# Optimization experiments

Hardware: AMD Instinct MI355X
Metric: run time of the kernel (lower is better)

The kernel has to match this reference:

```python
import jax, jax.numpy as jnp
import numpy as np

H = 16
D_MODEL = 1024
D_K = D_MODEL // H


def setup_inputs() -> dict:
    key = jax.random.key(0)
    ks = jax.random.split(key, 11)
    B, S = 2, 2048
    scale = 1.0 / np.sqrt(D_MODEL)
    inp = {
        "query": jax.random.normal(ks[0], (B, S, D_MODEL), dtype=jnp.float32),
        "key": jax.random.normal(ks[1], (B, S, D_MODEL), dtype=jnp.float32),
        "value": jax.random.normal(ks[2], (B, S, D_MODEL), dtype=jnp.float32),
        "Wq": jax.random.normal(ks[3], (D_MODEL, D_MODEL), dtype=jnp.float32) * scale,
        "bq": jnp.zeros((D_MODEL,), dtype=jnp.float32),
        "Wk": jax.random.normal(ks[4], (D_MODEL, D_MODEL), dtype=jnp.float32) * scale,
        "bk": jnp.zeros((D_MODEL,), dtype=jnp.float32),
        "Wv": jax.random.normal(ks[5], (D_MODEL, D_MODEL), dtype=jnp.float32) * scale,
        "bv": jnp.zeros((D_MODEL,), dtype=jnp.float32),
        "Wo": jax.random.normal(ks[6], (D_MODEL, D_MODEL), dtype=jnp.float32) * scale,
        "bo": jnp.zeros((D_MODEL,), dtype=jnp.float32),
    }
    return inp


def _mha(query, key, value, Wq, bq, Wk, bk, Wv, bv, Wo, bo):
    B, S, _ = query.shape
    # linear projections (torch nn.Linear: x @ W.T + b)
    q = query @ Wq.T + bq
    k = key @ Wk.T + bk
    v = value @ Wv.T + bv
    # split heads: [B, S, D] -> [B, H, S, d_k]
    q = q.reshape(B, S, H, D_K).transpose(0, 2, 1, 3)
    k = k.reshape(B, S, H, D_K).transpose(0, 2, 1, 3)
    v = v.reshape(B, S, H, D_K).transpose(0, 2, 1, 3)
    # scaled dot-product attention with manual stable softmax
    scores = jnp.einsum("bhqd,bhkd->bhqk", q, k) / jnp.sqrt(jnp.float32(D_K))
    stable = scores - jnp.max(scores, axis=-1, keepdims=True)
    e = jnp.exp(stable)
    attn = e / jnp.sum(e, axis=-1, keepdims=True)
    ctx = jnp.einsum("bhqk,bhkd->bhqd", attn, v)
    # merge heads and final projection
    ctx = ctx.transpose(0, 2, 1, 3).reshape(B, S, H * D_K)
    return ctx @ Wo.T + bo


def reference(query, key, value, Wq, bq, Wk, bk, Wv, bv, Wo, bo):
    return _mha(query, key, value, Wq, bq, Wk, bk, Wv, bv, Wo, bo)
```

## Files before the change

### kernel.cpp

```cpp
#include <hip/hip_runtime.h>


#define S_LEN 2048
#define BATCH 2
#define DM    1024
#define NH    16
#define DKH   64
#define BS    (BATCH * S_LEN)

typedef _Float16 f16x8 __attribute__((ext_vector_type(8)));
typedef _Float16 f16x4 __attribute__((ext_vector_type(4)));
typedef _Float16 f16x2 __attribute__((ext_vector_type(2)));
typedef __fp16   h16x2 __attribute__((ext_vector_type(2)));
typedef float    f32x4 __attribute__((ext_vector_type(4)));

__device__ __forceinline__ f16x2 pk_f16(float a, float b) {
  h16x2 r = __builtin_amdgcn_cvt_pkrtz(a, b);
  return __builtin_bit_cast(f16x2, r);
}

__device__ __forceinline__ void gld16(const void* g, void* l) {
  __builtin_amdgcn_global_load_lds(
      (const __attribute__((address_space(1))) void*)g,
      (__attribute__((address_space(3))) void*)l, 16, 0, 0);
}

__device__ __forceinline__ float fast_exp2(float x) {
#if __has_builtin(__builtin_amdgcn_exp2f)
  return __builtin_amdgcn_exp2f(x);
#else
  return exp2f(x);
#endif
}

__global__ __launch_bounds__(256) void cvt_all(
    const float* __restrict__ q, const float* __restrict__ k, const float* __restrict__ v,
    const float* __restrict__ wq, const float* __restrict__ wk,
    const float* __restrict__ wv, const float* __restrict__ wo,
    _Float16* __restrict__ xq, _Float16* __restrict__ xk, _Float16* __restrict__ xv,
    _Float16* __restrict__ w16)
{
  const int y = blockIdx.y;
  const float* src; _Float16* dst; int n;
  if (y == 0)      { src = q;  dst = xq; n = BS * DM; }
  else if (y == 1) { src = k;  dst = xk; n = BS * DM; }
  else if (y == 2) { src = v;  dst = xv; n = BS * DM; }
  else {
    src = (y == 3) ? wq : ((y == 4) ? wk : ((y == 5) ? wv : wo));
    dst = w16 + (size_t)(y - 3) * (DM * DM);
    n = DM * DM;
  }
  int i0 = (blockIdx.x * 256 + threadIdx.x) * 4;
  if (i0 < n) {
    float4 f = *(const float4*)(src + i0);
    f16x2 lo = pk_f16(f.x, f.y);
    f16x2 hi = pk_f16(f.z, f.w);
    f16x4 h; h[0] = lo[0]; h[1] = lo[1]; h[2] = hi[0]; h[3] = hi[1];
    *(f16x4*)(dst + i0) = h;
  }
}

template <typename OUT_T, bool VT>
__device__ __forceinline__ void gemm_core(
    const _Float16* __restrict__ A, const _Float16* __restrict__ W,
    const float* __restrict__ bias, OUT_T* __restrict__ out, float oscale)
{
  const int tid  = threadIdx.x;
  const int l    = tid & 63;
  const int wv   = tid >> 6;
  const int c    = l & 15, quad = l >> 4;
  const int m0   = blockIdx.y * 128, n0 = blockIdx.x * 128;
  const int wm   = wv & 1, wn = wv >> 1;
  __shared__ _Float16 sA[128 * 64];
  __shared__ _Float16 sB[128 * 64];

  const _Float16* gA[4]; const _Float16* gB[4];
#pragma unroll
  for (int p = 0; p < 4; ++p) {
    int s = tid + p * 256, r = s >> 3, g = (s & 7) ^ (r & 7);
    gA[p] = A + (size_t)(m0 + r) * DM + g * 8;
    gB[p] = W + (size_t)(n0 + r) * DM + g * 8;
  }
  const int cx = c & 7;

  f32x4 acc[4][4] = {};
  for (int k0 = 0; k0 < DM; k0 += 64) {
    __syncthreads();
#pragma unroll
    for (int p = 0; p < 4; ++p) {
      gld16(gA[p] + k0, sA + (tid + p * 256) * 8);
      gld16(gB[p] + k0, sB + (tid + p * 256) * 8);
    }
    __syncthreads();
#pragma unroll
    for (int ks = 0; ks < 2; ++ks) {
      f16x8 af[4], bf[4];
#pragma unroll
      for (int i = 0; i < 4; ++i)
        af[i] = *(const f16x8*)&sA[(wm * 64 + i * 16 + c) * 64 + ((ks * 4 + quad) ^ cx) * 8];
#pragma unroll
      for (int j = 0; j < 4; ++j)
        bf[j] = *(const f16x8*)&sB[(wn * 64 + j * 16 + c) * 64 + ((ks * 4 + quad) ^ cx) * 8];
#pragma unroll
      for (int i = 0; i < 4; ++i)
#pragma unroll
        for (int j = 0; j < 4; ++j)
          acc[i][j] = __builtin_amdgcn_mfma_f32_16x16x32_f16(af[i], bf[j], acc[i][j], 0, 0, 0);
    }
  }
  if constexpr (VT) {
#pragma unroll
    for (int j = 0; j < 4; ++j) {
      int col = n0 + wn * 64 + j * 16 + c;
      float bb = bias[col];
      int hh = col >> 6, dd = col & 63;
#pragma unroll
      for (int i = 0; i < 4; ++i) {
        int row = m0 + wm * 64 + i * 16 + quad * 4;
        int bb2 = row >> 11, ss = row & (S_LEN - 1);
        _Float16* dst = (_Float16*)out + ((size_t)(bb2 * NH + hh) * DKH + dd) * S_LEN + ss;
        f16x4 v4;
#pragma unroll
        for (int r = 0; r < 4; ++r) v4[r] = (_Float16)((acc[i][j][r] + bb) * oscale);
        *(f16x4*)dst = v4;
      }
    }
  } else {
#pragma unroll
    for (int j = 0; j < 4; ++j) {
      int col = n0 + wn * 64 + j * 16 + c;
      float bb = bias[col];
#pragma unroll
      for (int i = 0; i < 4; ++i) {
        int row = m0 + wm * 64 + i * 16 + quad * 4;
#pragma unroll
        for (int r = 0; r < 4; ++r) {
          float vv = (acc[i][j][r] + bb) * oscale;
          out[(size_t)(row + r) * DM + col] = (OUT_T)vv;
        }
      }
    }
  }
}

#define SC_Q (0.125f * 1.44269504088896340736f)

__global__ __launch_bounds__(256) void proj3(
    const _Float16* __restrict__ xq, const _Float16* __restrict__ xk,
    const _Float16* __restrict__ xv, const _Float16* __restrict__ w16,
    const float* __restrict__ bq, const float* __restrict__ bk, const float* __restrict__ bv,
    _Float16* __restrict__ Q, _Float16* __restrict__ K, _Float16* __restrict__ Vt)
{
  const int z = blockIdx.z;
  if (z == 2) {
    gemm_core<_Float16, true>(xv, w16 + (size_t)2 * DM * DM, bv, Vt, 1.0f);
  } else if (z == 0) {
    gemm_core<_Float16, false>(xq, w16, bq, Q, SC_Q);
  } else {
    gemm_core<_Float16, false>(xk, w16 + (size_t)DM * DM, bk, K, 1.0f);
  }
}

__global__ __launch_bounds__(256) void out_gemm(
    const _Float16* __restrict__ ctx, const _Float16* __restrict__ wo,
    const float* __restrict__ bo, float* __restrict__ out)
{
  gemm_core<float, false>(ctx, wo, bo, out, 1.0f);
}

#define APP 72
__global__ __launch_bounds__(256) void attn(
    const _Float16* __restrict__ Q, const _Float16* __restrict__ K,
    const _Float16* __restrict__ Vt, _Float16* __restrict__ ctx)
{
  const int tid = threadIdx.x;
  const int l   = tid & 63, wv = tid >> 6;
  const int c   = l & 15, quad = l >> 4;
  const int q0  = blockIdx.x * 64;
  const int bh  = blockIdx.y;
  const int b   = bh >> 4, h = bh & 15;
  const int wq  = wv & 1, wd = wv >> 1;
  __shared__ _Float16 sK[64 * 64];
  __shared__ _Float16 sV[64 * 64];
  __shared__ _Float16 sP[64 * APP];
  __shared__ float    lsum[64][4];

  f16x8 qf[4][2];
#pragma unroll
  for (int nt = 0; nt < 4; ++nt) {
    const _Float16* Qg = Q + ((size_t)(b * S_LEN + q0 + nt * 16 + c)) * DM + h * DKH;
    qf[nt][0] = *(const f16x8*)(Qg + quad * 8);
    qf[nt][1] = *(const f16x8*)(Qg + 32 + quad * 8);
  }

  f32x4 o[2][2] = {};
  float l_part[4] = {};

  const _Float16* Kg0 = K + ((size_t)b * S_LEN) * DM + h * DKH;
  const _Float16* Vg0 = Vt + ((size_t)bh * DKH) * S_LEN;

  const int sa = tid,       ra = sa >> 3, ba = (sa & 7) ^ (ra & 7);
  const int sb = tid + 256, rb = sb >> 3, bb = (sb & 7) ^ (rb & 7);
  const _Float16* gKa = Kg0 + (size_t)ra * DM + ba * 8;
  const _Float16* gKb = Kg0 + (size_t)rb * DM + bb * 8;
  const _Float16* gVa = Vg0 + (size_t)ra * S_LEN + ba * 8;
  const _Float16* gVb = Vg0 + (size_t)rb * S_LEN + bb * 8;
  const int cx = c & 7;

  for (int kt = 0; kt < S_LEN / 64; ++kt) {
    const int k0 = kt * 64;
    __syncthreads();
    gld16(gKa + (size_t)k0 * DM, sK + sa * 8);
    gld16(gKb + (size_t)k0 * DM, sK + sb * 8);
    gld16(gVa + k0,              sV + sa * 8);
    gld16(gVb + k0,              sV + sb * 8);
    __syncthreads();

    f32x4 sAcc[4] = {};
#pragma unroll
    for (int ks = 0; ks < 2; ++ks) {
      f16x8 kf = *(const f16x8*)&sK[(wv * 16 + c) * 64 + ((ks * 4 + quad) ^ cx) * 8];
#pragma unroll
      for (int nt = 0; nt < 4; ++nt)
        sAcc[nt] = __builtin_amdgcn_mfma_f32_16x16x32_f16(kf, qf[nt][ks], sAcc[nt], 0, 0, 0);
    }

#pragma unroll
    for (int nt = 0; nt < 4; ++nt) {
      float p0 = fast_exp2(sAcc[nt][0]);
      float p1 = fast_exp2(sAcc[nt][1]);
      float p2 = fast_exp2(sAcc[nt][2]);
      float p3 = fast_exp2(sAcc[nt][3]);
      l_part[nt] += (p0 + p1) + (p2 + p3);
      f16x2 lo = pk_f16(p0, p1);
      f16x2 hi = pk_f16(p2, p3);
      f16x4 pk; pk[0] = lo[0]; pk[1] = lo[1]; pk[2] = hi[0]; pk[3] = hi[1];
      *(f16x4*)&sP[(nt * 16 + c) * APP + wv * 16 + quad * 4] = pk;
    }
    __syncthreads();

#pragma unroll
    for (int ks = 0; ks < 2; ++ks) {
      f16x8 af[2], bf[2];
#pragma unroll
      for (int qb = 0; qb < 2; ++qb)
        af[qb] = *(const f16x8*)&sP[(wq * 32 + qb * 16 + c) * APP + ks * 32 + quad * 8];
#pragma unroll
      for (int db = 0; db < 2; ++db)
        bf[db] = *(const f16x8*)&sV[(wd * 32 + db * 16 + c) * 64 + ((ks * 4 + quad) ^ cx) * 8];
#pragma unroll
      for (int qb = 0; qb < 2; ++qb)
#pragma unroll
        for (int db = 0; db < 2; ++db)
          o[qb][db] = __builtin_amdgcn_mfma_f32_16x16x32_f16(af[qb], bf[db], o[qb][db], 0, 0, 0);
    }
  }

#pragma unroll
  for (int nt = 0; nt < 4; ++nt) {
    float s = l_part[nt];
    s += __shfl_xor(s, 16);
    s += __shfl_xor(s, 32);
    l_part[nt] = s;
  }
  if (quad == 0) {
#pragma unroll
    for (int nt = 0; nt < 4; ++nt) lsum[nt * 16 + c][wv] = l_part[nt];
  }
  __syncthreads();

#pragma unroll
  for (int qb = 0; qb < 2; ++qb) {
#pragma unroll
    for (int r = 0; r < 4; ++r) {
      int q = wq * 32 + qb * 16 + quad * 4 + r;
      f32x4 ls = *(const f32x4*)&lsum[q][0];
      float inv = 1.0f / (ls[0] + ls[1] + ls[2] + ls[3]);
      _Float16* Og = ctx + ((size_t)(b * S_LEN + q0 + q)) * DM + h * DKH;
#pragma unroll
      for (int db = 0; db < 2; ++db)
        Og[wd * 32 + db * 16 + c] = (_Float16)(o[qb][db][r] * inv);
    }
  }
}

extern "C" void kernel_launch(void* const* d_in, const int* in_sizes, int n_in,
                              void* d_out, int out_size, void* d_ws, size_t ws_size,
                              hipStream_t stream)
{
  (void)in_sizes; (void)n_in; (void)out_size; (void)ws_size;
  const float* q  = (const float*)d_in[0];
  const float* k  = (const float*)d_in[1];
  const float* v  = (const float*)d_in[2];
  const float* wq = (const float*)d_in[3];
  const float* bq = (const float*)d_in[4];
  const float* wk = (const float*)d_in[5];
  const float* bk = (const float*)d_in[6];
  const float* wv = (const float*)d_in[7];
  const float* bv = (const float*)d_in[8];
  const float* wo = (const float*)d_in[9];
  const float* bo = (const float*)d_in[10];

  char* ws = (char*)d_ws;
  _Float16* XQ  = (_Float16*)(ws);
  _Float16* XK  = (_Float16*)(ws + (8u  << 20));
  _Float16* XV  = (_Float16*)(ws + (16u << 20));
  _Float16* W16 = (_Float16*)(ws + (24u << 20));
  _Float16* Qp  = (_Float16*)(ws + (32u << 20));
  _Float16* Kp  = (_Float16*)(ws + (40u << 20));
  _Float16* VT  = (_Float16*)(ws + (48u << 20));
  _Float16* CTX = XQ;
  float* out = (float*)d_out;

  cvt_all<<<dim3(4096, 7), 256, 0, stream>>>(q, k, v, wq, wk, wv, wo, XQ, XK, XV, W16);
  proj3<<<dim3(8, 32, 3), 256, 0, stream>>>(XQ, XK, XV, W16, bq, bk, bv, Qp, Kp, VT);
  attn<<<dim3(32, 32), 256, 0, stream>>>(Qp, Kp, VT, CTX);
  out_gemm<<<dim3(8, 32), 256, 0, stream>>>(CTX, W16 + (size_t)3 * DM * DM, bo, out);
}
```

Measured before the change: 240.1 us.

## Double-buffer K/V tiles in attention and swizzle the P buffer

Adds a second LDS buffer for K and V so the next tile's async global-to-LDS loads are issued before computing on the current tile, overlapping memory latency with MFMA work. The P scratch buffer drops its padding in favour of an XOR swizzle, the row-sum accumulation switches to fdot2 on the packed f16 probabilities, and lsum reuses the K buffer. It also adds a min-blocks launch bound to raise occupancy. The cost is more LDS per block and register pressure from the occupancy hint. The row sums are now taken from f16-rounded probabilities, matching what is multiplied with V.

```diff
diff --git a/kernel.cpp b/kernel.cpp
--- a/kernel.cpp
+++ b/kernel.cpp
@@ -168,8 +168,7 @@
   gemm_core<float, false>(ctx, wo, bo, out, 1.0f);
 }
 
-#define APP 72
-__global__ __launch_bounds__(256) void attn(
+__global__ __launch_bounds__(256, 4) void attn(
     const _Float16* __restrict__ Q, const _Float16* __restrict__ K,
     const _Float16* __restrict__ Vt, _Float16* __restrict__ ctx)
 {
@@ -180,10 +179,9 @@
   const int bh  = blockIdx.y;
   const int b   = bh >> 4, h = bh & 15;
   const int wq  = wv & 1, wd = wv >> 1;
-  __shared__ _Float16 sK[64 * 64];
-  __shared__ _Float16 sV[64 * 64];
-  __shared__ _Float16 sP[64 * APP];
-  __shared__ float    lsum[64][4];
+  __shared__ _Float16 sK[2][64 * 64];
+  __shared__ _Float16 sV[2][64 * 64];
+  __shared__ _Float16 sP[64 * 64];
 
   f16x8 qf[4][2];
 #pragma unroll
@@ -195,6 +193,7 @@
 
   f32x4 o[2][2] = {};
   float l_part[4] = {};
+  const f16x2 ones = {(_Float16)1.0f, (_Float16)1.0f};
 
   const _Float16* Kg0 = K + ((size_t)b * S_LEN) * DM + h * DKH;
   const _Float16* Vg0 = Vt + ((size_t)bh * DKH) * S_LEN;
@@ -207,19 +206,25 @@
   const _Float16* gVb = Vg0 + (size_t)rb * S_LEN + bb * 8;
   const int cx = c & 7;
 
+  gld16(gKa, sK[0] + sa * 8);
+  gld16(gKb, sK[0] + sb * 8);
+  gld16(gVa, sV[0] + sa * 8);
+  gld16(gVb, sV[0] + sb * 8);
+  __syncthreads();
+
   for (int kt = 0; kt < S_LEN / 64; ++kt) {
-    const int k0 = kt * 64;
-    __syncthreads();
-    gld16(gKa + (size_t)k0 * DM, sK + sa * 8);
-    gld16(gKb + (size_t)k0 * DM, sK + sb * 8);
-    gld16(gVa + k0,              sV + sa * 8);
-    gld16(gVb + k0,              sV + sb * 8);
-    __syncthreads();
+    const int cur = kt & 1;
+    const int nk = (kt < S_LEN / 64 - 1) ? (kt + 1) : kt;
+    const size_t k0n = (size_t)nk * 64;
+    gld16(gKa + k0n * DM, sK[cur ^ 1] + sa * 8);
+    gld16(gKb + k0n * DM, sK[cur ^ 1] + sb * 8);
+    gld16(gVa + k0n,      sV[cur ^ 1] + sa * 8);
+    gld16(gVb + k0n,      sV[cur ^ 1] + sb * 8);
 
     f32x4 sAcc[4] = {};
 #pragma unroll
     for (int ks = 0; ks < 2; ++ks) {
-      f16x8 kf = *(const f16x8*)&sK[(wv * 16 + c) * 64 + ((ks * 4 + quad) ^ cx) * 8];
+      f16x8 kf = *(const f16x8*)&sK[cur][(wv * 16 + c) * 64 + ((ks * 4 + quad) ^ cx) * 8];
 #pragma unroll
       for (int nt = 0; nt < 4; ++nt)
         sAcc[nt] = __builtin_amdgcn_mfma_f32_16x16x32_f16(kf, qf[nt][ks], sAcc[nt], 0, 0, 0);
@@ -231,11 +236,16 @@
       float p1 = fast_exp2(sAcc[nt][1]);
       float p2 = fast_exp2(sAcc[nt][2]);
       float p3 = fast_exp2(sAcc[nt][3]);
-      l_part[nt] += (p0 + p1) + (p2 + p3);
       f16x2 lo = pk_f16(p0, p1);
       f16x2 hi = pk_f16(p2, p3);
+      l_part[nt] = __builtin_amdgcn_fdot2(__builtin_bit_cast(h16x2, lo),
+                                          __builtin_bit_cast(h16x2, ones), l_part[nt], false);
+      l_part[nt] = __builtin_amdgcn_fdot2(__builtin_bit_cast(h16x2, hi),
+                                          __builtin_bit_cast(h16x2, ones), l_part[nt], false);
       f16x4 pk; pk[0] = lo[0]; pk[1] = lo[1]; pk[2] = hi[0]; pk[3] = hi[1];
-      *(f16x4*)&sP[(nt * 16 + c) * APP + wv * 16 + quad * 4] = pk;
+      int row = nt * 16 + c;
+      int blk = (wv * 2 + (quad >> 1)) ^ (row & 7);
+      *(f16x4*)&sP[row * 64 + blk * 8 + (quad & 1) * 4] = pk;
     }
     __syncthreads();
 
@@ -243,17 +253,20 @@
     for (int ks = 0; ks < 2; ++ks) {
       f16x8 af[2], bf[2];
 #pragma unroll
-      for (int qb = 0; qb < 2; ++qb)
-        af[qb] = *(const f16x8*)&sP[(wq * 32 + qb * 16 + c) * APP + ks * 32 + quad * 8];
+      for (int qb = 0; qb < 2; ++qb) {
+        int row = wq * 32 + qb * 16 + c;
+        af[qb] = *(const f16x8*)&sP[row * 64 + ((ks * 4 + quad) ^ (row & 7)) * 8];
+      }
 #pragma unroll
       for (int db = 0; db < 2; ++db)
-        bf[db] = *(const f16x8*)&sV[(wd * 32 + db * 16 + c) * 64 + ((ks * 4 + quad) ^ cx) * 8];
+        bf[db] = *(const f16x8*)&sV[cur][(wd * 32 + db * 16 + c) * 64 + ((ks * 4 + quad) ^ cx) * 8];
 #pragma unroll
       for (int qb = 0; qb < 2; ++qb)
 #pragma unroll
         for (int db = 0; db < 2; ++db)
           o[qb][db] = __builtin_amdgcn_mfma_f32_16x16x32_f16(af[qb], bf[db], o[qb][db], 0, 0, 0);
     }
+    __syncthreads();
   }
 
 #pragma unroll
@@ -263,9 +276,10 @@
     s += __shfl_xor(s, 32);
     l_part[nt] = s;
   }
+  float* lsum = (float*)&sK[0][0];
   if (quad == 0) {
 #pragma unroll
-    for (int nt = 0; nt < 4; ++nt) lsum[nt * 16 + c][wv] = l_part[nt];
+    for (int nt = 0; nt < 4; ++nt) lsum[(nt * 16 + c) * 4 + wv] = l_part[nt];
   }
   __syncthreads();
 
@@ -274,7 +288,7 @@
 #pragma unroll
     for (int r = 0; r < 4; ++r) {
       int q = wq * 32 + qb * 16 + quad * 4 + r;
-      f32x4 ls = *(const f32x4*)&lsum[q][0];
+      f32x4 ls = *(const f32x4*)&lsum[q * 4];
       float inv = 1.0f / (ls[0] + ls[1] + ls[2] + ls[3]);
       _Float16* Og = ctx + ((size_t)(b * S_LEN + q0 + q)) * DM + h * DKH;
 #pragma unroll
```

Result: faster. 234.3 us (-2.4%).
